# Kernel tuning notes

Hardware: AMD Instinct MI355X
Metric: run time of the kernel (lower is better)

Reference implementation:

```python
import jax, jax.numpy as jnp
import numpy as np

B, D = 8, 256
N_LIVE, K_NEW = 10000, 32
KC = N_LIVE + K_NEW
N_SAMPLES = 100
EPSILON = 0.1


def setup_inputs() -> dict:
    key = jax.random.key(0)
    k1, k2, k3, k4, k5, k6 = jax.random.split(key, 6)
    return {
        "xt": jax.random.normal(k1, (B, D), dtype=jnp.float32),
        "live_x0": jax.random.normal(k2, (B, N_LIVE, D), dtype=jnp.float32),
        "live_ll": jax.random.normal(k3, (B, N_LIVE, 1), dtype=jnp.float32),
        "x0": jax.random.normal(k4, (B, K_NEW, D), dtype=jnp.float32),
        "ll": jax.random.normal(k5, (B, K_NEW, 1), dtype=jnp.float32),
        "t_scale": jnp.float32(0.5),
        "boot_idx": jax.random.randint(k6, (N_SAMPLES, B, KC), 0, KC, dtype=jnp.int32),
    }


def reference(xt, live_x0, live_ll, x0, ll, t_scale, boot_idx):
    # --- spotlight_score core math ---
    # gaussian correction for the new particles: 0.5*||x0-xt||^2/sigma^2 + log(sigma)
    diff_new = x0 - xt[:, None, :]                                   # [B,K,D]
    corr_new = 0.5 * jnp.sum(diff_new ** 2, axis=-1, keepdims=True) / t_scale ** 2  # [B,K,1]
    current_x0 = jnp.concatenate([live_x0, x0], axis=1)              # [B,Kc,D]
    current_ll = jnp.concatenate(
        [live_ll, ll + corr_new + jnp.log(t_scale)], axis=1)         # [B,Kc,1]

    diff = current_x0 - xt[:, None, :]                               # [B,Kc,D]
    use_ll = (current_ll
              - 0.5 * jnp.sum(diff ** 2, axis=-1, keepdims=True) / t_scale ** 2
              - jnp.log(t_scale))                                    # [B,Kc,1]

    scores_p = diff / t_scale                                        # [B,Kc,D] per-particle scores
    logits = use_ll[..., 0]                                          # [B,Kc]

    # --- check_convergence: bootstrap resampled softmax reductions ---
    def body(carry, idx_n):                                          # idx_n: [B,Kc]
        s = jnp.take_along_axis(scores_p, idx_n[:, :, None], axis=1)  # [B,Kc,D]
        l = jnp.take_along_axis(logits, idx_n, axis=1)                # [B,Kc]
        w = jax.nn.softmax(l, axis=1)
        return carry, jnp.einsum('bk,bkd->bd', w, s)                  # [B,D]

    _, boot = jax.lax.scan(body, None, boot_idx)                      # [N,B,D]
    sigma_v = jnp.std(boot, axis=0, ddof=1)                           # [B,D] (torch.std is unbiased)
    converged = jnp.all(sigma_v < EPSILON * t_scale, axis=1)          # [B]

    # --- final importance-weighted score ---
    w = jax.nn.softmax(logits, axis=1)                                # [B,Kc]
    score = jnp.einsum('bk,bkd->bd', w, scores_p)                     # [B,D]
    return score, converged
```

## Files before the change

kernel.cpp:

```cpp
#include <hip/hip_runtime.h>
#include <math.h>

#define B 8
#define D 256
#define N_LIVE 10000
#define K_NEW 32
#define KC 10032
#define KC4 2508
#define NS 100
#define NROW 101
#define EPS 0.1f
#define CAPA 255
#define ACT_CUT 87.0f
#define LBLK 314
#define BMAX_STRIDE 320

#define WS_BMAX   0
#define WS_LOGITS (WS_BMAX + B * BMAX_STRIDE)
#define WS_BOOT   (WS_LOGITS + B * KC)


__global__ __launch_bounds__(256) void k_logits(
    const float* __restrict__ xt, const float* __restrict__ live_x0,
    const float* __restrict__ live_ll, const float* __restrict__ x0n,
    const float* __restrict__ lln, const float* __restrict__ ts_p,
    float* __restrict__ logits, float* __restrict__ bmax) {
  int b = blockIdx.y;
  int w = threadIdx.x >> 6;
  int lane = threadIdx.x & 63;
  int k0 = blockIdx.x * 32 + w * 8;
  bool valid = (k0 < KC);
  int kb = valid ? k0 : 0;
  float4 c = ((const float4*)(xt + b * D))[lane];

  float s[8];
#pragma unroll
  for (int p = 0; p < 8; p++) {
    int k = kb + p;
    const float* src = (k < N_LIVE)
        ? (live_x0 + ((size_t)b * N_LIVE + k) * D)
        : (x0n + ((size_t)b * K_NEW + (k - N_LIVE)) * D);
    float4 v = ((const float4*)src)[lane];
    float dx = v.x - c.x, dy = v.y - c.y, dz = v.z - c.z, dw = v.w - c.w;
    s[p] = dx * dx + dy * dy + dz * dz + dw * dw;
  }
#pragma unroll
  for (int off = 32; off; off >>= 1) {
#pragma unroll
    for (int p = 0; p < 8; p++) s[p] += __shfl_xor(s[p], off);
  }
  __shared__ float wlog[4];
  if (lane == 0) {
    float ts = *ts_p;
    float inv2 = 0.5f / (ts * ts), lts = logf(ts);
    float o[8];
#pragma unroll
    for (int p = 0; p < 8; p++) {
      int k = kb + p;
      o[p] = (k < N_LIVE)
          ? live_ll[(size_t)b * N_LIVE + k] - s[p] * inv2 - lts
          : lln[(size_t)b * K_NEW + (k - N_LIVE)];
    }
    if (valid) {
      float4 o0 = {o[0], o[1], o[2], o[3]}, o1 = {o[4], o[5], o[6], o[7]};
      *(float4*)(logits + (size_t)b * KC + kb) = o0;
      *(float4*)(logits + (size_t)b * KC + kb + 4) = o1;
      wlog[w] = fmaxf(fmaxf(fmaxf(o[0], o[1]), fmaxf(o[2], o[3])),
                      fmaxf(fmaxf(o[4], o[5]), fmaxf(o[6], o[7])));
    } else {
      wlog[w] = -INFINITY;
    }
  }
  __syncthreads();
  if (threadIdx.x == 0)
    bmax[b * BMAX_STRIDE + blockIdx.x] =
        fmaxf(fmaxf(wlog[0], wlog[1]), fmaxf(wlog[2], wlog[3]));
}

__global__ __launch_bounds__(256) void k_boot(
    const float* __restrict__ live_x0, const float* __restrict__ x0n,
    const float* __restrict__ logits, const float* __restrict__ bmax,
    const int* __restrict__ boot_idx, float* __restrict__ boot) {
  int n = blockIdx.x;
  int b = blockIdx.y;
  int tid = threadIdx.x;
  int nw = tid >> 6, lane = tid & 63;
  __shared__ unsigned slut32[KC4];
  __shared__ float se[CAPA + 1];
  __shared__ int sidx[CAPA + 1];
  __shared__ int cnt[CAPA + 1];
  __shared__ float4 part[4][64];
  __shared__ float sred[4];
  __shared__ int sacnt;

  float m = -INFINITY;
  for (int i = tid; i < LBLK; i += 256) m = fmaxf(m, bmax[b * BMAX_STRIDE + i]);
#pragma unroll
  for (int off = 32; off; off >>= 1) m = fmaxf(m, __shfl_xor(m, off));
  if (lane == 0) sred[nw] = m;
  if (tid == 0) sacnt = 0;

  int4 pre[10];
  if (n < NS) {
    const int4* brow = (const int4*)(boot_idx + ((size_t)n * B + b) * KC);
#pragma unroll
    for (int i = 0; i < 10; i++) {
      int k4 = tid + i * 256;
      if (k4 < KC4) pre[i] = brow[k4];
    }
  }
  __syncthreads();
  float M = fmaxf(fmaxf(sred[0], sred[1]), fmaxf(sred[2], sred[3]));
  float thr = M - ACT_CUT;

  const float4* lg4 = (const float4*)(logits + (size_t)b * KC);
  cnt[tid] = (n < NS) ? 0 : 1;
#pragma unroll
  for (int i = 0; i < 10; i++) {
    int k4 = tid + i * 256;
    if (k4 < KC4) {
      float4 l4 = lg4[k4];
      unsigned pack = 0;
      float le; int pos;
      le = l4.x; if (le > thr) { pos = atomicAdd(&sacnt, 1); if (pos < CAPA) {
          se[pos] = expf(le - M); sidx[pos] = 4 * k4;     pack |= (unsigned)(pos + 1); } }
      le = l4.y; if (le > thr) { pos = atomicAdd(&sacnt, 1); if (pos < CAPA) {
          se[pos] = expf(le - M); sidx[pos] = 4 * k4 + 1; pack |= (unsigned)(pos + 1) << 8; } }
      le = l4.z; if (le > thr) { pos = atomicAdd(&sacnt, 1); if (pos < CAPA) {
          se[pos] = expf(le - M); sidx[pos] = 4 * k4 + 2; pack |= (unsigned)(pos + 1) << 16; } }
      le = l4.w; if (le > thr) { pos = atomicAdd(&sacnt, 1); if (pos < CAPA) {
          se[pos] = expf(le - M); sidx[pos] = 4 * k4 + 3; pack |= (unsigned)(pos + 1) << 24; } }
      slut32[k4] = pack;
    }
  }
  __syncthreads();
  int A = min(sacnt, CAPA);

  const unsigned char* lutb = (const unsigned char*)slut32;
  if (n < NS) {
#pragma unroll
    for (int i = 0; i < 10; i++) {
      int k4 = tid + i * 256;
      if (k4 < KC4) {
        int4 v = pre[i];
        int t;
        t = lutb[v.x]; if (t) atomicAdd(&cnt[t - 1], 1);
        t = lutb[v.y]; if (t) atomicAdd(&cnt[t - 1], 1);
        t = lutb[v.z]; if (t) atomicAdd(&cnt[t - 1], 1);
        t = lutb[v.w]; if (t) atomicAdd(&cnt[t - 1], 1);
      }
    }
  }
  __syncthreads();

  float d = (tid < A) ? (float)cnt[tid] * se[tid] : 0.f;
#pragma unroll
  for (int off = 32; off; off >>= 1) d += __shfl_xor(d, off);
  if (lane == 0) sred[nw] = d;
  __syncthreads();
  float inv = 1.f / (sred[0] + sred[1] + sred[2] + sred[3]);

  const float* lx = live_x0 + (size_t)b * N_LIVE * D;
  const float* nx = x0n + (size_t)b * K_NEW * D;
  float4 a0 = {0.f, 0.f, 0.f, 0.f};
  for (int p = nw; p < A; p += 4) {
    int c = cnt[p];
    if (!c) continue;
    float w = (float)c * se[p];
    int j = sidx[p];
    const float4* r = (const float4*)((j < N_LIVE) ? (lx + (size_t)j * D)
                                                   : (nx + (size_t)(j - N_LIVE) * D));
    float4 v = r[lane];
    a0.x = fmaf(w, v.x, a0.x); a0.y = fmaf(w, v.y, a0.y);
    a0.z = fmaf(w, v.z, a0.z); a0.w = fmaf(w, v.w, a0.w);
  }
  part[nw][lane] = a0;
  __syncthreads();
  if (nw == 0) {
    float4 q0 = part[0][lane], q1 = part[1][lane], q2 = part[2][lane], q3 = part[3][lane];
    float4 r;
    r.x = ((q0.x + q1.x) + (q2.x + q3.x)) * inv;
    r.y = ((q0.y + q1.y) + (q2.y + q3.y)) * inv;
    r.z = ((q0.z + q1.z) + (q2.z + q3.z)) * inv;
    r.w = ((q0.w + q1.w) + (q2.w + q3.w)) * inv;
    ((float4*)(boot + ((size_t)b * NROW + n) * D))[lane] = r;
  }
}

__global__ __launch_bounds__(1024) void k_final(
    const float* __restrict__ boot, const float* __restrict__ xt,
    const float* __restrict__ ts_p, float* __restrict__ out) {
  int b = blockIdx.x;
  int tid = threadIdx.x;
  int d = tid & 255;
  int st = tid >> 8;
  float ts = *ts_p;
  const float* bb = boot + (size_t)b * NROW * D + d;
  __shared__ float red[4][256];
  __shared__ float mrow[256];
  __shared__ int wok[4];
  float s = 0.f;
#pragma unroll 5
  for (int i = 0; i < 25; i++) s += bb[(size_t)(st + 4 * i) * D];
  red[st][d] = s;
  __syncthreads();
  if (st == 0) mrow[d] = (red[0][d] + red[1][d] + red[2][d] + red[3][d]) / (float)NS;
  __syncthreads();
  float mean = mrow[d];
  float vs = 0.f;
#pragma unroll 5
  for (int i = 0; i < 25; i++) {
    float t = bb[(size_t)(st + 4 * i) * D] - mean;
    vs += t * t;
  }
  red[st][d] = vs;
  __syncthreads();
  if (st == 0) {
    float var = (red[0][d] + red[1][d] + red[2][d] + red[3][d]) / (float)(NS - 1);
    float sigma_raw = sqrtf(var);
    bool ok = (sigma_raw / ts) < (EPS * ts);
    out[(size_t)b * D + d] = (bb[(size_t)NS * D] - xt[(size_t)b * D + d]) / ts;
    unsigned long long mba = __ballot(ok);
    if ((d & 63) == 0) wok[d >> 6] = (mba == 0xFFFFFFFFFFFFFFFFull) ? 1 : 0;
  }
  __syncthreads();
  if (tid == 0)
    out[(size_t)B * D + b] = (wok[0] & wok[1] & wok[2] & wok[3]) ? 1.0f : 0.0f;
}

extern "C" void kernel_launch(void* const* d_in, const int* in_sizes, int n_in,
                              void* d_out, int out_size, void* d_ws, size_t ws_size,
                              hipStream_t stream) {
  const float* xt       = (const float*)d_in[0];
  const float* live_x0  = (const float*)d_in[1];
  const float* live_ll  = (const float*)d_in[2];
  const float* x0n      = (const float*)d_in[3];
  const float* lln      = (const float*)d_in[4];
  const float* ts_p     = (const float*)d_in[5];
  const int*   boot_idx = (const int*)d_in[6];
  float* out = (float*)d_out;
  float* ws  = (float*)d_ws;

  float* bmax   = ws + WS_BMAX;
  float* logits = ws + WS_LOGITS;
  float* boot   = ws + WS_BOOT;

  k_logits<<<dim3(LBLK, B), 256, 0, stream>>>(xt, live_x0, live_ll, x0n, lln, ts_p, logits, bmax);
  k_boot<<<dim3(NROW, B), 256, 0, stream>>>(live_x0, x0n, logits, bmax, boot_idx, boot);
  k_final<<<dim3(B), 1024, 0, stream>>>(boot, xt, ts_p, out);
}
```

Baseline: 170.5 us.

## Fuse final std/convergence reduction into boot kernel via last-block counter

Removes the separate k_final launch by having each k_boot block atomically increment a per-batch done counter. The last block to finish for each batch computes the mean, variance, convergence flag and final score. The counter is reset inside k_logits. This saves one kernel launch and its gap, but adds threadfences and an atomic per block, and the final reduction now runs in one 256-thread block per batch instead of 1024 threads.

Result: slower. 225.6 us (+32.3%).

```diff
diff --git a/kernel.cpp b/kernel.cpp
--- a/kernel.cpp
+++ b/kernel.cpp
@@ -18,14 +18,17 @@
 #define WS_BMAX   0
 #define WS_LOGITS (WS_BMAX + B * BMAX_STRIDE)
 #define WS_BOOT   (WS_LOGITS + B * KC)
+#define WS_DONE   (WS_BOOT + B * NROW * D)
 
 
 __global__ __launch_bounds__(256) void k_logits(
     const float* __restrict__ xt, const float* __restrict__ live_x0,
     const float* __restrict__ live_ll, const float* __restrict__ x0n,
     const float* __restrict__ lln, const float* __restrict__ ts_p,
-    float* __restrict__ logits, float* __restrict__ bmax) {
+    float* __restrict__ logits, float* __restrict__ bmax,
+    unsigned* __restrict__ done) {
   int b = blockIdx.y;
+  if (blockIdx.x == 0 && threadIdx.x == 0) done[b] = 0;
   int w = threadIdx.x >> 6;
   int lane = threadIdx.x & 63;
   int k0 = blockIdx.x * 32 + w * 8;
@@ -80,7 +83,9 @@
 __global__ __launch_bounds__(256) void k_boot(
     const float* __restrict__ live_x0, const float* __restrict__ x0n,
     const float* __restrict__ logits, const float* __restrict__ bmax,
-    const int* __restrict__ boot_idx, float* __restrict__ boot) {
+    const int* __restrict__ boot_idx, float* __restrict__ boot,
+    unsigned* __restrict__ done, const float* __restrict__ xt,
+    const float* __restrict__ ts_p, float* __restrict__ out) {
   int n = blockIdx.x;
   int b = blockIdx.y;
   int tid = threadIdx.x;
@@ -92,6 +97,7 @@
   __shared__ float4 part[4][64];
   __shared__ float sred[4];
   __shared__ int sacnt;
+  __shared__ int slast;
 
   float m = -INFINITY;
   for (int i = tid; i < LBLK; i += 256) m = fmaxf(m, bmax[b * BMAX_STRIDE + i]);
@@ -153,10 +159,10 @@
   }
   __syncthreads();
 
-  float d = (tid < A) ? (float)cnt[tid] * se[tid] : 0.f;
-#pragma unroll
-  for (int off = 32; off; off >>= 1) d += __shfl_xor(d, off);
-  if (lane == 0) sred[nw] = d;
+  float dnum = (tid < A) ? (float)cnt[tid] * se[tid] : 0.f;
+#pragma unroll
+  for (int off = 32; off; off >>= 1) dnum += __shfl_xor(dnum, off);
+  if (lane == 0) sred[nw] = dnum;
   __syncthreads();
   float inv = 1.f / (sred[0] + sred[1] + sred[2] + sred[3]);
 
@@ -185,44 +191,43 @@
     r.w = ((q0.w + q1.w) + (q2.w + q3.w)) * inv;
     ((float4*)(boot + ((size_t)b * NROW + n) * D))[lane] = r;
   }
-}
-
-__global__ __launch_bounds__(1024) void k_final(
-    const float* __restrict__ boot, const float* __restrict__ xt,
-    const float* __restrict__ ts_p, float* __restrict__ out) {
-  int b = blockIdx.x;
-  int tid = threadIdx.x;
-  int d = tid & 255;
-  int st = tid >> 8;
+
+  __threadfence();
+  __syncthreads();
+  if (tid == 0) slast = (atomicAdd(&done[b], 1) == NROW - 1) ? 1 : 0;
+  __syncthreads();
+  if (!slast) return;
+  __threadfence();
+
+  int d = tid;
   float ts = *ts_p;
   const float* bb = boot + (size_t)b * NROW * D + d;
-  __shared__ float red[4][256];
-  __shared__ float mrow[256];
+  float s0 = 0.f, s1 = 0.f, s2 = 0.f, s3 = 0.f;
+#pragma unroll 4
+  for (int i = 0; i < NS; i += 4) {
+    s0 += bb[(size_t)(i) * D];
+    s1 += bb[(size_t)(i + 1) * D];
+    s2 += bb[(size_t)(i + 2) * D];
+    s3 += bb[(size_t)(i + 3) * D];
+  }
+  float mean = ((s0 + s1) + (s2 + s3)) / (float)NS;
+  float v0 = 0.f, v1 = 0.f, v2 = 0.f, v3 = 0.f;
+#pragma unroll 4
+  for (int i = 0; i < NS; i += 4) {
+    float t0 = bb[(size_t)(i) * D] - mean;
+    float t1 = bb[(size_t)(i + 1) * D] - mean;
+    float t2 = bb[(size_t)(i + 2) * D] - mean;
+    float t3 = bb[(size_t)(i + 3) * D] - mean;
+    v0 = fmaf(t0, t0, v0); v1 = fmaf(t1, t1, v1);
+    v2 = fmaf(t2, t2, v2); v3 = fmaf(t3, t3, v3);
+  }
+  float var = ((v0 + v1) + (v2 + v3)) / (float)(NS - 1);
+  float sigma_raw = sqrtf(var);
+  bool ok = (sigma_raw / ts) < (EPS * ts);
+  out[(size_t)b * D + d] = (bb[(size_t)NS * D] - xt[(size_t)b * D + d]) / ts;
+  unsigned long long mba = __ballot(ok);
   __shared__ int wok[4];
-  float s = 0.f;
-#pragma unroll 5
-  for (int i = 0; i < 25; i++) s += bb[(size_t)(st + 4 * i) * D];
-  red[st][d] = s;
-  __syncthreads();
-  if (st == 0) mrow[d] = (red[0][d] + red[1][d] + red[2][d] + red[3][d]) / (float)NS;
-  __syncthreads();
-  float mean = mrow[d];
-  float vs = 0.f;
-#pragma unroll 5
-  for (int i = 0; i < 25; i++) {
-    float t = bb[(size_t)(st + 4 * i) * D] - mean;
-    vs += t * t;
-  }
-  red[st][d] = vs;
-  __syncthreads();
-  if (st == 0) {
-    float var = (red[0][d] + red[1][d] + red[2][d] + red[3][d]) / (float)(NS - 1);
-    float sigma_raw = sqrtf(var);
-    bool ok = (sigma_raw / ts) < (EPS * ts);
-    out[(size_t)b * D + d] = (bb[(size_t)NS * D] - xt[(size_t)b * D + d]) / ts;
-    unsigned long long mba = __ballot(ok);
-    if ((d & 63) == 0) wok[d >> 6] = (mba == 0xFFFFFFFFFFFFFFFFull) ? 1 : 0;
-  }
+  if (lane == 0) wok[nw] = (mba == 0xFFFFFFFFFFFFFFFFull) ? 1 : 0;
   __syncthreads();
   if (tid == 0)
     out[(size_t)B * D + b] = (wok[0] & wok[1] & wok[2] & wok[3]) ? 1.0f : 0.0f;
@@ -241,11 +246,11 @@
   float* out = (float*)d_out;
   float* ws  = (float*)d_ws;
 
-  float* bmax   = ws + WS_BMAX;
-  float* logits = ws + WS_LOGITS;
-  float* boot   = ws + WS_BOOT;
-
-  k_logits<<<dim3(LBLK, B), 256, 0, stream>>>(xt, live_x0, live_ll, x0n, lln, ts_p, logits, bmax);
-  k_boot<<<dim3(NROW, B), 256, 0, stream>>>(live_x0, x0n, logits, bmax, boot_idx, boot);
-  k_final<<<dim3(B), 1024, 0, stream>>>(boot, xt, ts_p, out);
+  float* bmax    = ws + WS_BMAX;
+  float* logits  = ws + WS_LOGITS;
+  float* boot    = ws + WS_BOOT;
+  unsigned* done = (unsigned*)(ws + WS_DONE);
+
+  k_logits<<<dim3(LBLK, B), 256, 0, stream>>>(xt, live_x0, live_ll, x0n, lln, ts_p, logits, bmax, done);
+  k_boot<<<dim3(NROW, B), 256, 0, stream>>>(live_x0, x0n, logits, bmax, boot_idx, boot, done, xt, ts_p, out);
 }
```

## Hoist active-set selection into a separate kernel and fast-path the new-only case

Applied to the files above, without the earlier changes.

A new k_select kernel computes the per-batch max, thresholds the logits, and writes the compacted active list, exp weights and a byte LUT to workspace once. Before, every one of the 101 bootstrap blocks per batch redid this work. k_boot now reads the precomputed data and runs with 512 threads. When no live particle passes the cutoff, it takes a fast path that counts only indices at or above N_LIVE and skips the LUT load. This adds a kernel launch and global-memory round trips for the LUT. The fast path rests on the premise that live logits are heavily penalised by the distance term.

Result: no change. 169.3 us (-0.7%).

```diff
diff --git a/kernel.cpp b/kernel.cpp
--- a/kernel.cpp
+++ b/kernel.cpp
@@ -10,22 +10,29 @@
 #define NS 100
 #define NROW 101
 #define EPS 0.1f
+#define CAP 256
 #define CAPA 255
 #define ACT_CUT 87.0f
 #define LBLK 314
 #define BMAX_STRIDE 320
 
-#define WS_BMAX   0
+#define WS_HDR    0
+#define WS_BMAX   160
 #define WS_LOGITS (WS_BMAX + B * BMAX_STRIDE)
-#define WS_BOOT   (WS_LOGITS + B * KC)
+#define WS_ACTE   (WS_LOGITS + B * KC)
+#define WS_ACTI   (WS_ACTE + B * CAP)
+#define WS_LUT    (WS_ACTI + B * CAP)
+#define WS_BOOT   (WS_LUT + B * KC / 4)
 
 
 __global__ __launch_bounds__(256) void k_logits(
     const float* __restrict__ xt, const float* __restrict__ live_x0,
     const float* __restrict__ live_ll, const float* __restrict__ x0n,
     const float* __restrict__ lln, const float* __restrict__ ts_p,
-    float* __restrict__ logits, float* __restrict__ bmax) {
+    float* __restrict__ logits, float* __restrict__ bmax,
+    unsigned* __restrict__ hdr) {
   int b = blockIdx.y;
+  if (blockIdx.x == 0 && threadIdx.x == 0) { hdr[b] = 0; hdr[8 + b] = 0; }
   int w = threadIdx.x >> 6;
   int lane = threadIdx.x & 63;
   int k0 = blockIdx.x * 32 + w * 8;
@@ -77,77 +84,117 @@
         fmaxf(fmaxf(wlog[0], wlog[1]), fmaxf(wlog[2], wlog[3]));
 }
 
-__global__ __launch_bounds__(256) void k_boot(
+__global__ __launch_bounds__(256) void k_select(
+    const float* __restrict__ logits, const float* __restrict__ bmax,
+    unsigned* __restrict__ hdr, float* __restrict__ act_e,
+    int* __restrict__ act_idx, unsigned char* __restrict__ lut) {
+  int b = blockIdx.y;
+  __shared__ float sm[4];
+  float m = -INFINITY;
+  for (int i = threadIdx.x; i < LBLK; i += 256)
+    m = fmaxf(m, bmax[b * BMAX_STRIDE + i]);
+#pragma unroll
+  for (int off = 32; off; off >>= 1) m = fmaxf(m, __shfl_xor(m, off));
+  if ((threadIdx.x & 63) == 0) sm[threadIdx.x >> 6] = m;
+  __syncthreads();
+  float M = fmaxf(fmaxf(sm[0], sm[1]), fmaxf(sm[2], sm[3]));
+  if (blockIdx.x == 0 && threadIdx.x == 0) hdr[16 + b] = __float_as_uint(M);
+  float thr = M - ACT_CUT;
+
+  int tid = blockIdx.x * 256 + threadIdx.x;
+  const float* lg = logits + (size_t)b * KC;
+  unsigned* cnt = &hdr[b];
+  for (int k = tid; k < KC; k += 8 * 256) {
+    float l = lg[k];
+    unsigned char v = 0;
+    if (l > thr) {
+      if (k < N_LIVE) atomicOr(&hdr[8 + b], 1u);
+      int pos = (int)atomicAdd(cnt, 1u);
+      if (pos < CAPA) {
+        act_e[b * CAP + pos] = expf(l - M);
+        act_idx[b * CAP + pos] = k;
+        v = (unsigned char)(pos + 1);
+      }
+    }
+    lut[(size_t)b * KC + k] = v;
+  }
+}
+
+__global__ __launch_bounds__(512) void k_boot(
     const float* __restrict__ live_x0, const float* __restrict__ x0n,
-    const float* __restrict__ logits, const float* __restrict__ bmax,
-    const int* __restrict__ boot_idx, float* __restrict__ boot) {
+    const float* __restrict__ logits, const unsigned* __restrict__ hdr,
+    const float* __restrict__ act_e, const int* __restrict__ act_idx,
+    const unsigned char* __restrict__ lut, const int* __restrict__ boot_idx,
+    float* __restrict__ boot) {
   int n = blockIdx.x;
   int b = blockIdx.y;
   int tid = threadIdx.x;
   int nw = tid >> 6, lane = tid & 63;
   __shared__ unsigned slut32[KC4];
-  __shared__ float se[CAPA + 1];
-  __shared__ int sidx[CAPA + 1];
-  __shared__ int cnt[CAPA + 1];
-  __shared__ float4 part[4][64];
-  __shared__ float sred[4];
-  __shared__ int sacnt;
-
-  float m = -INFINITY;
-  for (int i = tid; i < LBLK; i += 256) m = fmaxf(m, bmax[b * BMAX_STRIDE + i]);
-#pragma unroll
-  for (int off = 32; off; off >>= 1) m = fmaxf(m, __shfl_xor(m, off));
-  if (lane == 0) sred[nw] = m;
-  if (tid == 0) sacnt = 0;
-
-  int4 pre[10];
+  __shared__ float se[CAP];
+  __shared__ int sidx[CAP];
+  __shared__ int cnt[CAP];
+  __shared__ float4 part[8][64];
+  __shared__ float sred[8];
+
+  int flag = (int)hdr[8 + b];
+  float M = __uint_as_float(hdr[16 + b]);
+  int A;
+
+  int4 pre[5];
   if (n < NS) {
     const int4* brow = (const int4*)(boot_idx + ((size_t)n * B + b) * KC);
 #pragma unroll
-    for (int i = 0; i < 10; i++) {
-      int k4 = tid + i * 256;
+    for (int i = 0; i < 5; i++) {
+      int k4 = tid + i * 512;
       if (k4 < KC4) pre[i] = brow[k4];
     }
   }
-  __syncthreads();
-  float M = fmaxf(fmaxf(sred[0], sred[1]), fmaxf(sred[2], sred[3]));
-  float thr = M - ACT_CUT;
-
-  const float4* lg4 = (const float4*)(logits + (size_t)b * KC);
-  cnt[tid] = (n < NS) ? 0 : 1;
-#pragma unroll
-  for (int i = 0; i < 10; i++) {
-    int k4 = tid + i * 256;
-    if (k4 < KC4) {
-      float4 l4 = lg4[k4];
-      unsigned pack = 0;
-      float le; int pos;
-      le = l4.x; if (le > thr) { pos = atomicAdd(&sacnt, 1); if (pos < CAPA) {
-          se[pos] = expf(le - M); sidx[pos] = 4 * k4;     pack |= (unsigned)(pos + 1); } }
-      le = l4.y; if (le > thr) { pos = atomicAdd(&sacnt, 1); if (pos < CAPA) {
-          se[pos] = expf(le - M); sidx[pos] = 4 * k4 + 1; pack |= (unsigned)(pos + 1) << 8; } }
-      le = l4.z; if (le > thr) { pos = atomicAdd(&sacnt, 1); if (pos < CAPA) {
-          se[pos] = expf(le - M); sidx[pos] = 4 * k4 + 2; pack |= (unsigned)(pos + 1) << 16; } }
-      le = l4.w; if (le > thr) { pos = atomicAdd(&sacnt, 1); if (pos < CAPA) {
-          se[pos] = expf(le - M); sidx[pos] = 4 * k4 + 3; pack |= (unsigned)(pos + 1) << 24; } }
-      slut32[k4] = pack;
-    }
-  }
-  __syncthreads();
-  int A = min(sacnt, CAPA);
-
-  const unsigned char* lutb = (const unsigned char*)slut32;
-  if (n < NS) {
-#pragma unroll
-    for (int i = 0; i < 10; i++) {
-      int k4 = tid + i * 256;
-      if (k4 < KC4) {
-        int4 v = pre[i];
-        int t;
-        t = lutb[v.x]; if (t) atomicAdd(&cnt[t - 1], 1);
-        t = lutb[v.y]; if (t) atomicAdd(&cnt[t - 1], 1);
-        t = lutb[v.z]; if (t) atomicAdd(&cnt[t - 1], 1);
-        t = lutb[v.w]; if (t) atomicAdd(&cnt[t - 1], 1);
+
+  if (flag == 0) {
+    A = K_NEW;
+    if (tid < K_NEW) {
+      se[tid] = expf(logits[(size_t)b * KC + N_LIVE + tid] - M);
+      sidx[tid] = N_LIVE + tid;
+      cnt[tid] = (n < NS) ? 0 : 1;
+    }
+    __syncthreads();
+    if (n < NS) {
+#pragma unroll
+      for (int i = 0; i < 5; i++) {
+        int k4 = tid + i * 512;
+        if (k4 < KC4) {
+          int4 v = pre[i];
+          if (v.x >= N_LIVE) atomicAdd(&cnt[v.x - N_LIVE], 1);
+          if (v.y >= N_LIVE) atomicAdd(&cnt[v.y - N_LIVE], 1);
+          if (v.z >= N_LIVE) atomicAdd(&cnt[v.z - N_LIVE], 1);
+          if (v.w >= N_LIVE) atomicAdd(&cnt[v.w - N_LIVE], 1);
+        }
+      }
+    }
+  } else {
+    A = min((int)hdr[b], CAPA);
+    for (int i = tid; i < A; i += 512) {
+      se[i] = act_e[b * CAP + i];
+      sidx[i] = act_idx[b * CAP + i];
+      cnt[i] = (n < NS) ? 0 : 1;
+    }
+    const unsigned* gl = (const unsigned*)(lut + (size_t)b * KC);
+    for (int i = tid; i < KC4; i += 512) slut32[i] = gl[i];
+    __syncthreads();
+    const unsigned char* lutb = (const unsigned char*)slut32;
+    if (n < NS) {
+#pragma unroll
+      for (int i = 0; i < 5; i++) {
+        int k4 = tid + i * 512;
+        if (k4 < KC4) {
+          int4 v = pre[i];
+          int t;
+          t = lutb[v.x]; if (t) atomicAdd(&cnt[t - 1], 1);
+          t = lutb[v.y]; if (t) atomicAdd(&cnt[t - 1], 1);
+          t = lutb[v.z]; if (t) atomicAdd(&cnt[t - 1], 1);
+          t = lutb[v.w]; if (t) atomicAdd(&cnt[t - 1], 1);
+        }
       }
     }
   }
@@ -158,12 +205,13 @@
   for (int off = 32; off; off >>= 1) d += __shfl_xor(d, off);
   if (lane == 0) sred[nw] = d;
   __syncthreads();
-  float inv = 1.f / (sred[0] + sred[1] + sred[2] + sred[3]);
+  float inv = 1.f / (((sred[0] + sred[1]) + (sred[2] + sred[3])) +
+                     ((sred[4] + sred[5]) + (sred[6] + sred[7])));
 
   const float* lx = live_x0 + (size_t)b * N_LIVE * D;
   const float* nx = x0n + (size_t)b * K_NEW * D;
   float4 a0 = {0.f, 0.f, 0.f, 0.f};
-  for (int p = nw; p < A; p += 4) {
+  for (int p = nw; p < A; p += 8) {
     int c = cnt[p];
     if (!c) continue;
     float w = (float)c * se[p];
@@ -177,12 +225,15 @@
   part[nw][lane] = a0;
   __syncthreads();
   if (nw == 0) {
-    float4 q0 = part[0][lane], q1 = part[1][lane], q2 = part[2][lane], q3 = part[3][lane];
+    float4 q0 = part[0][lane], q1 = part[1][lane];
+    float4 q2 = part[2][lane], q3 = part[3][lane];
+    float4 q4 = part[4][lane], q5 = part[5][lane];
+    float4 q6 = part[6][lane], q7 = part[7][lane];
     float4 r;
-    r.x = ((q0.x + q1.x) + (q2.x + q3.x)) * inv;
-    r.y = ((q0.y + q1.y) + (q2.y + q3.y)) * inv;
-    r.z = ((q0.z + q1.z) + (q2.z + q3.z)) * inv;
-    r.w = ((q0.w + q1.w) + (q2.w + q3.w)) * inv;
+    r.x = (((q0.x + q1.x) + (q2.x + q3.x)) + ((q4.x + q5.x) + (q6.x + q7.x))) * inv;
+    r.y = (((q0.y + q1.y) + (q2.y + q3.y)) + ((q4.y + q5.y) + (q6.y + q7.y))) * inv;
+    r.z = (((q0.z + q1.z) + (q2.z + q3.z)) + ((q4.z + q5.z) + (q6.z + q7.z))) * inv;
+    r.w = (((q0.w + q1.w) + (q2.w + q3.w)) + ((q4.w + q5.w) + (q6.w + q7.w))) * inv;
     ((float4*)(boot + ((size_t)b * NROW + n) * D))[lane] = r;
   }
 }
@@ -241,11 +292,16 @@
   float* out = (float*)d_out;
   float* ws  = (float*)d_ws;
 
-  float* bmax   = ws + WS_BMAX;
-  float* logits = ws + WS_LOGITS;
-  float* boot   = ws + WS_BOOT;
-
-  k_logits<<<dim3(LBLK, B), 256, 0, stream>>>(xt, live_x0, live_ll, x0n, lln, ts_p, logits, bmax);
-  k_boot<<<dim3(NROW, B), 256, 0, stream>>>(live_x0, x0n, logits, bmax, boot_idx, boot);
+  unsigned* hdr       = (unsigned*)(ws + WS_HDR);
+  float* bmax         = ws + WS_BMAX;
+  float* logits       = ws + WS_LOGITS;
+  float* act_e        = ws + WS_ACTE;
+  int*   act_idx      = (int*)(ws + WS_ACTI);
+  unsigned char* lut  = (unsigned char*)(ws + WS_LUT);
+  float* boot         = ws + WS_BOOT;
+
+  k_logits<<<dim3(LBLK, B), 256, 0, stream>>>(xt, live_x0, live_ll, x0n, lln, ts_p, logits, bmax, hdr);
+  k_select<<<dim3(8, B), 256, 0, stream>>>(logits, bmax, hdr, act_e, act_idx, lut);
+  k_boot<<<dim3(NROW, B), 512, 0, stream>>>(live_x0, x0n, logits, hdr, act_e, act_idx, lut, boot_idx, boot);
   k_final<<<dim3(B), 1024, 0, stream>>>(boot, xt, ts_p, out);
 }
```
